# Kernel optimization log

Measured on AMD Instinct MI355X. Metric: run time of the kernel, lower is better.

Reference implementation:

```python
import jax, jax.numpy as jnp
import numpy as np

O, T, DIN, H, DOUT = 50000, 500000, 128, 256, 128


def setup_inputs() -> dict:
    key = jax.random.key(0)
    ks = jax.random.split(key, 12)
    s = 0.05
    return {
        "obj_vecs": jax.random.normal(ks[0], (O, DIN), jnp.float32),
        "pred_vecs": jax.random.normal(ks[1], (T, DIN), jnp.float32),
        "edges": jax.random.randint(ks[2], (T, 2), 0, O, jnp.int64),
        "w1a": jax.random.normal(ks[3], (3 * DIN, H), jnp.float32) * s,
        "b1a": jax.random.normal(ks[4], (H,), jnp.float32) * s,
        "w1b": jax.random.normal(ks[5], (H, 2 * H + DOUT), jnp.float32) * s,
        "b1b": jax.random.normal(ks[6], (2 * H + DOUT,), jnp.float32) * s,
        "w2a": jax.random.normal(ks[7], (H, H), jnp.float32) * s,
        "b2a": jax.random.normal(ks[8], (H,), jnp.float32) * s,
        "w2b": jax.random.normal(ks[9], (H, DOUT), jnp.float32) * s,
        "b2b": jax.random.normal(ks[10], (DOUT,), jnp.float32) * s,
    }


def reference(obj_vecs, pred_vecs, edges, w1a, b1a, w1b, b1b, w2a, b2a, w2b, b2b):
    n_obj = obj_vecs.shape[0]
    h_dim = w2a.shape[0]
    d_out = w2b.shape[1]
    s_idx = edges[:, 0]
    o_idx = edges[:, 1]
    # gather subject/object node features, concat with predicate: [T, 3*Din]
    cur_t = jnp.concatenate([obj_vecs[s_idx], pred_vecs, obj_vecs[o_idx]], axis=1)
    # edge MLP (net1): Linear-ReLU-Linear-ReLU -> [T, 2H + Dout]
    new_t = jax.nn.relu(jax.nn.relu(cur_t @ w1a + b1a) @ w1b + b1b)
    new_s = new_t[:, :h_dim]
    new_p = new_t[:, h_dim:h_dim + d_out]
    new_o = new_t[:, h_dim + d_out:]
    # scatter-add pooling back to nodes, both endpoints
    idx = jnp.concatenate([s_idx, o_idx])
    vals = jnp.concatenate([new_s, new_o], axis=0)
    pooled = jax.ops.segment_sum(vals, idx, num_segments=n_obj)
    # avg pooling: divide by per-node incidence count (clamped to >= 1)
    counts = jax.ops.segment_sum(jnp.ones(idx.shape[0], obj_vecs.dtype), idx,
                                 num_segments=n_obj)
    pooled = pooled / jnp.clip(counts, 1.0)[:, None]
    # node MLP (net2)
    new_obj = jax.nn.relu(jax.nn.relu(pooled @ w2a + b2a) @ w2b + b2b)
    return new_obj, new_p
```

## Files before the change

kernel.cpp:

```cpp
#include <hip/hip_runtime.h>


using f32x4 = __attribute__((ext_vector_type(4))) float;
using s16x8 = __attribute__((ext_vector_type(8))) short;
typedef unsigned short u16x8 __attribute__((ext_vector_type(8)));

#define VMCNT4  asm volatile("s_waitcnt vmcnt(4)" ::: "memory")
#define VMCNT8  asm volatile("s_waitcnt vmcnt(8)" ::: "memory")
#define VMCNT16 asm volatile("s_waitcnt vmcnt(16)" ::: "memory")
#define VMCNT20 asm volatile("s_waitcnt vmcnt(20)" ::: "memory")
#define VMCNT36 asm volatile("s_waitcnt vmcnt(36)" ::: "memory")
#define LGKM0   asm volatile("s_waitcnt lgkmcnt(0)" ::: "memory")
#define BAR     __builtin_amdgcn_s_barrier()
#define SCHEDB  __builtin_amdgcn_sched_barrier(0)

static __device__ __forceinline__ unsigned short f2b(float f) {
    unsigned int u = __float_as_uint(f);
    unsigned int r = (u + 0x7fffu + ((u >> 16) & 1u)) >> 16;
    return (unsigned short)r;
}

static __device__ __forceinline__ unsigned f2bpk(float lo, float hi) {
    unsigned r;
    asm("v_cvt_pk_bf16_f32 %0, %1, %2" : "=v"(r) : "v"(lo), "v"(hi));
    return r;
}

static __device__ __forceinline__ float b2f(unsigned short b) {
    return __uint_as_float(((unsigned)b) << 16);
}

static __device__ __forceinline__ unsigned swz(unsigned row, unsigned byteoff) {
    return byteoff ^ ((row & 7u) << 4);
}

static __device__ __forceinline__ void gload_lds16(const unsigned short* g, unsigned short* l) {
    __builtin_amdgcn_global_load_lds(
        (const __attribute__((address_space(1))) unsigned int*)g,
        (__attribute__((address_space(3))) unsigned int*)l,
        16, 0, 0);
}

#define PREP_ELEMS (98304 + 163840 + 65536 + 32768)

__global__ void prep_count_kernel(const float* __restrict__ w1a, const float* __restrict__ w1b,
                                  const float* __restrict__ w2a, const float* __restrict__ w2b,
                                  unsigned short* __restrict__ w1aT, unsigned short* __restrict__ w1bT,
                                  unsigned short* __restrict__ w2aT, unsigned short* __restrict__ w2bT,
                                  const int* __restrict__ edges, int* __restrict__ cnt,
                                  int* __restrict__ slotS, int* __restrict__ slotO, int T) {
    int t = blockIdx.x * blockDim.x + threadIdx.x;
    if (t >= PREP_ELEMS) {
        int e = t - PREP_ELEMS;
        if (e < T) {
            slotS[e] = atomicAdd(&cnt[edges[2 * (long long)e]], 1);
            slotO[e] = atomicAdd(&cnt[edges[2 * (long long)e + 1]], 1);
        }
        return;
    }
    if (t < 6 * 16384) {
        int kt = t >> 14;
        int rem = t & 16383; int c = rem >> 6, kk = rem & 63;
        unsigned byte = ((unsigned)(c * 128 + kk * 2)) ^ ((c & 7u) << 4);
        *(unsigned short*)((char*)w1aT + (size_t)kt * 32768 + byte) =
            f2b(w1a[(size_t)(kt * 64 + kk) * 256 + c]);
        return;
    }
    t -= 98304;
    if (t < 10 * 16384) {
        int tile = t >> 14; int nc = tile >> 1, kh = tile & 1;
        int rem = t & 16383; int c = rem >> 7, kk = rem & 127;
        unsigned byte = ((unsigned)(c * 256 + kk * 2)) ^ ((c & 7u) << 4);
        *(unsigned short*)((char*)w1bT + (size_t)tile * 32768 + byte) =
            f2b(w1b[(size_t)(kh * 128 + kk) * 640 + nc * 128 + c]);
        return;
    }
    t -= 163840;
    if (t < 65536) { int n = t >> 8, k = t & 255; w2aT[t] = f2b(w2a[k * 256 + n]); return; }
    t -= 65536;
    if (t < 32768) { int n = t >> 8, k = t & 255; w2bT[t] = f2b(w2b[k * 128 + n]); return; }
}

__global__ void scan_kernel(const int* __restrict__ cnt, int* __restrict__ rowptr, int O) {
    __shared__ int sc[1024];
    const int tid = threadIdx.x;
    const int per = (O + 1023) >> 10;
    const int base = tid * per;
    int s = 0;
    for (int i = 0; i < per; ++i) { int j = base + i; if (j < O) s += cnt[j]; }
    sc[tid] = s;
    __syncthreads();
    for (int d = 1; d < 1024; d <<= 1) {
        int v = (tid >= d) ? sc[tid - d] : 0;
        __syncthreads();
        sc[tid] += v;
        __syncthreads();
    }
    int off = sc[tid] - s;
    for (int i = 0; i < per; ++i) {
        int j = base + i;
        if (j < O) { rowptr[j] = off; off += cnt[j]; }
    }
    if (tid == 0) rowptr[O] = sc[1023];
}

__global__ __launch_bounds__(512, 2) void edge_mlp(
    const float* __restrict__ obj, const float* __restrict__ pred,
    const int* __restrict__ edges,
    const unsigned short* __restrict__ w1aT, const float* __restrict__ b1a,
    const unsigned short* __restrict__ w1bT, const float* __restrict__ b1b,
    const int* __restrict__ slotS, const int* __restrict__ slotO,
    const int* __restrict__ rowptr,
    unsigned short* __restrict__ edgeout, float* __restrict__ outP, int T) {
    const int m0 = blockIdx.x * 128;
    const int tid = threadIdx.x;
    const int lane = tid & 63, wid = tid >> 6;
    const int wm = wid >> 2, wn = wid & 3;
    const bool evenL = ((lane & 1) == 0);

    __shared__ unsigned short U[81920];
    char* const ldsb = (char*)U;
    char* const bbase = ldsb + 65536;

    bool okR[4][4];
    #pragma unroll
    for (int mi = 0; mi < 4; ++mi)
        #pragma unroll
        for (int rr = 0; rr < 4; ++rr)
            okR[mi][rr] = (m0 + wm * 64 + mi * 16 + ((lane >> 4) << 2) + rr) < T;

    int slotSr[4][2], slotOr[4][2];
    #pragma unroll
    for (int mi = 0; mi < 4; ++mi)
        #pragma unroll
        for (int k = 0; k < 2; ++k) {
            int rsel = evenL ? k : 2 + k;
            int e = m0 + wm * 64 + mi * 16 + ((lane >> 4) << 2) + rsel;
            if (e >= T) e = T - 1;
            int si = edges[2 * (long long)e];
            int oi = edges[2 * (long long)e + 1];
            slotSr[mi][k] = slotS[e] + rowptr[si];
            slotOr[mi][k] = slotO[e] + rowptr[oi];
        }

    const int r = tid >> 2;
    const int q = tid & 3;
    int e_r = m0 + r; if (e_r >= T) e_r = T - 1;
    const int sIdx_r = edges[2 * (long long)e_r];
    const int oIdx_r = edges[2 * (long long)e_r + 1];

    float bias1[4], bias2[5][2];
    #pragma unroll
    for (int nj = 0; nj < 4; ++nj) bias1[nj] = b1a[wn * 64 + nj * 16 + (lane & 15)];
    #pragma unroll
    for (int nc = 0; nc < 5; ++nc)
        #pragma unroll
        for (int nj = 0; nj < 2; ++nj)
            bias2[nc][nj] = b1b[nc * 128 + wn * 32 + nj * 16 + (lane & 15)];

    #pragma unroll
    for (int mi = 0; mi < 4; ++mi)
        #pragma unroll
        for (int k = 0; k < 2; ++k)
            asm volatile("" :: "v"(slotSr[mi][k]), "v"(slotOr[mi][k]));
    #pragma unroll
    for (int nj = 0; nj < 4; ++nj) asm volatile("" :: "v"(bias1[nj]));
    #pragma unroll
    for (int nc = 0; nc < 5; ++nc)
        #pragma unroll
        for (int nj = 0; nj < 2; ++nj) asm volatile("" :: "v"(bias2[nc][nj]));
    asm volatile("" :: "v"((float)sIdx_r), "v"((float)oIdx_r));
    SCHEDB;

    auto aSrc = [&](int kt) -> const float4* {
        const float* s;
        if (kt < 2)      s = obj  + (long long)sIdx_r * 128 + kt * 64;
        else if (kt < 4) s = pred + (long long)e_r   * 128 + (kt - 2) * 64;
        else             s = obj  + (long long)oIdx_r * 128 + (kt - 4) * 64;
        return (const float4*)s;
    };

    auto tp = [&](int i) -> const unsigned short* {
        return (i < 6) ? (w1aT + (size_t)i * 16384) : (w1bT + (size_t)(i - 6) * 16384);
    };

    auto stage32 = [&](const unsigned short* gt, char* bb) {
        #pragma unroll
        for (int rr4 = 0; rr4 < 4; ++rr4) {
            unsigned off = wid * 4096u + rr4 * 1024u;
            gload_lds16((const unsigned short*)((const char*)gt + off + lane * 16u),
                        (unsigned short*)(bb + off));
        }
    };

    auto writeA = [&](const float4* ap, char* ab) {
        #pragma unroll
        for (int i = 0; i < 4; ++i) {
            float4 v = ap[i];
            uint2 pk;
            pk.x = f2bpk(v.x, v.y);
            pk.y = f2bpk(v.z, v.w);
            unsigned byte = (r * 128u + q * 32u + i * 8u) ^ ((r & 7u) << 4);
            *(uint2*)(ab + byte) = pk;
        }
    };

    f32x4 acc1[4][4];
    #pragma unroll
    for (int a = 0; a < 4; ++a)
        #pragma unroll
        for (int b = 0; b < 4; ++b) acc1[a][b] = f32x4{0.f, 0.f, 0.f, 0.f};

    auto mfma1 = [&](const char* ab, const char* bb) {
        #pragma unroll
        for (int ks = 0; ks < 2; ++ks) {
            const unsigned kk = ks * 32u + ((lane >> 4) << 3);
            s16x8 af[4];
            #pragma unroll
            for (int mi = 0; mi < 4; ++mi) {
                unsigned row = wm * 64u + mi * 16u + (lane & 15);
                af[mi] = *(const s16x8*)(ab + ((row * 128u + kk * 2u) ^ ((row & 7u) << 4)));
            }
            #pragma unroll
            for (int nj = 0; nj < 4; ++nj) {
                unsigned c = wn * 64u + nj * 16u + (lane & 15);
                s16x8 bf = *(const s16x8*)(bb + ((c * 128u + kk * 2u) ^ ((c & 7u) << 4)));
                #pragma unroll
                for (int mi = 0; mi < 4; ++mi)
                    acc1[mi][nj] = __builtin_amdgcn_mfma_f32_16x16x32_bf16(af[mi], bf, acc1[mi][nj], 0, 0, 0);
            }
        }
    };

    float4 ap[4];
    {
        const float4* s4 = aSrc(0);
        #pragma unroll
        for (int i = 0; i < 4; ++i) ap[i] = s4[q * 4 + i];
    }
    writeA(ap, ldsb);
    stage32(tp(0), bbase);
    stage32(tp(1), bbase + 32768);
    {
        const float4* s4 = aSrc(1);
        #pragma unroll
        for (int i = 0; i < 4; ++i) ap[i] = s4[q * 4 + i];
    }
    VMCNT8;
    LGKM0; BAR; SCHEDB;

    #pragma unroll
    for (int s = 0; s < 6; ++s) {
        stage32(tp(s + 2), bbase + ((s + 2) % 3) * 32768);
        __builtin_amdgcn_s_setprio(1);
        mfma1(ldsb + (s & 1) * 16384, bbase + (s % 3) * 32768);
        __builtin_amdgcn_s_setprio(0);
        VMCNT4;
        if (s < 5) {
            writeA(ap, ldsb + ((s + 1) & 1) * 16384);
            if (s < 4) {
                const float4* s4 = aSrc(s + 2);
                #pragma unroll
                for (int i = 0; i < 4; ++i) ap[i] = s4[q * 4 + i];
            }
        }
        LGKM0; BAR; SCHEDB;
    }

    #pragma unroll
    for (int nj = 0; nj < 4; ++nj) {
        unsigned col = wn * 64u + nj * 16u + (lane & 15);
        #pragma unroll
        for (int mi = 0; mi < 4; ++mi) {
            float r0 = fmaxf(acc1[mi][nj][0] + bias1[nj], 0.f);
            float r1 = fmaxf(acc1[mi][nj][1] + bias1[nj], 0.f);
            float r2 = fmaxf(acc1[mi][nj][2] + bias1[nj], 0.f);
            float r3 = fmaxf(acc1[mi][nj][3] + bias1[nj], 0.f);
            unsigned p01 = f2bpk(r0, r1);
            unsigned p23 = f2bpk(r2, r3);
            unsigned rowb = wm * 64u + mi * 16u + ((lane >> 4) << 2);
            *(unsigned short*)(ldsb + ((rowb * 512u + col * 2u) ^ ((rowb & 7u) << 4))) = (unsigned short)p01;
            *(unsigned short*)(ldsb + (((rowb + 1) * 512u + col * 2u) ^ (((rowb + 1) & 7u) << 4))) = (unsigned short)(p01 >> 16);
            *(unsigned short*)(ldsb + (((rowb + 2) * 512u + col * 2u) ^ (((rowb + 2) & 7u) << 4))) = (unsigned short)p23;
            *(unsigned short*)(ldsb + (((rowb + 3) * 512u + col * 2u) ^ (((rowb + 3) & 7u) << 4))) = (unsigned short)(p23 >> 16);
        }
    }
    LGKM0; BAR; SCHEDB;

    #pragma unroll
    for (int nc = 0; nc < 5; ++nc) {
        f32x4 acc2[4][2];
        #pragma unroll
        for (int a = 0; a < 4; ++a)
            #pragma unroll
            for (int b = 0; b < 2; ++b) acc2[a][b] = f32x4{0.f, 0.f, 0.f, 0.f};

        #pragma unroll
        for (int kh = 0; kh < 2; ++kh) {
            const int s = 6 + nc * 2 + kh;
            if (s + 2 <= 15) stage32(tp(s + 2), bbase + ((s + 2) % 3) * 32768);
            const char* bb = bbase + (s % 3) * 32768;
            __builtin_amdgcn_s_setprio(1);
            #pragma unroll
            for (int ks = 0; ks < 4; ++ks) {
                const unsigned kkB = ks * 32u + ((lane >> 4) << 3);
                const unsigned kkH = (kh * 128u) + kkB;
                s16x8 af[4];
                #pragma unroll
                for (int mi = 0; mi < 4; ++mi) {
                    unsigned row = wm * 64u + mi * 16u + (lane & 15);
                    af[mi] = *(const s16x8*)(ldsb + ((row * 512u + kkH * 2u) ^ ((row & 7u) << 4)));
                }
                #pragma unroll
                for (int nj = 0; nj < 2; ++nj) {
                    unsigned c = wn * 32u + nj * 16u + (lane & 15);
                    s16x8 bf = *(const s16x8*)(bb + ((c * 256u + kkB * 2u) ^ ((c & 7u) << 4)));
                    #pragma unroll
                    for (int mi = 0; mi < 4; ++mi)
                        acc2[mi][nj] = __builtin_amdgcn_mfma_f32_16x16x32_bf16(af[mi], bf, acc2[mi][nj], 0, 0, 0);
                }
            }
            __builtin_amdgcn_s_setprio(0);

            if (kh == 0) {
                if (s == 6)       { VMCNT4; }
                else if (s == 12) { VMCNT36; }
                else if (s == 14) { VMCNT16; }
                else              { VMCNT20; }
                LGKM0; BAR; SCHEDB;
            }
        }

        if (nc == 2) {
            #pragma unroll
            for (int nj = 0; nj < 2; ++nj) {
                int col = 2 * 128 + wn * 32 + nj * 16 + (lane & 15);
                #pragma unroll
                for (int mi = 0; mi < 4; ++mi)
                    #pragma unroll
                    for (int rr = 0; rr < 4; ++rr) {
                        int row = wm * 64 + mi * 16 + ((lane >> 4) << 2) + rr;
                        if (okR[mi][rr]) {
                            float v = acc2[mi][nj][rr] + bias2[2][nj];
                            v = v > 0.f ? v : 0.f;
                            outP[(long long)(m0 + row) * 128 + (col - 256)] = v;
                        }
                    }
            }
            VMCNT36;
            LGKM0; BAR; SCHEDB;
        } else {
            #pragma unroll
            for (int nj = 0; nj < 2; ++nj) {
                int col = nc * 128 + wn * 32 + nj * 16 + (lane & 15);
                int pc = (nc < 2) ? col : (col - 384);
                int pcb = (lane & 1) ? (pc - 1) : pc;
                #pragma unroll
                for (int mi = 0; mi < 4; ++mi) {
                    float vv[4];
                    #pragma unroll
                    for (int rr = 0; rr < 4; ++rr) {
                        float v = acc2[mi][nj][rr] + bias2[nc][nj];
                        vv[rr] = v > 0.f ? v : 0.f;
                    }
                    float nb0 = __shfl_xor(vv[0], 1);
                    float nb1 = __shfl_xor(vv[1], 1);
                    float nb2 = __shfl_xor(vv[2], 1);
                    float nb3 = __shfl_xor(vv[3], 1);
                    #pragma unroll
                    for (int k = 0; k < 2; ++k) {
                        float lo = evenL ? (k ? vv[1] : vv[0]) : (k ? nb3 : nb2);
                        float hi = evenL ? (k ? nb1 : nb0) : (k ? vv[3] : vv[2]);
                        int rsel = evenL ? k : 2 + k;
                        if (okR[mi][rsel]) {
                            int slot = (nc < 2) ? slotSr[mi][k] : slotOr[mi][k];
                            unsigned pk = f2bpk(lo, hi);
                            *(unsigned*)(edgeout + (size_t)slot * 256 + pcb) = pk;
                        }
                    }
                }
            }
            if (nc < 4) {
                VMCNT20;
                LGKM0; BAR; SCHEDB;
            }
        }
    }
}

__global__ __launch_bounds__(256, 3) void obj_mlp(
    const unsigned short* __restrict__ edgeout, const int* __restrict__ rowptr,
    const unsigned short* __restrict__ w2aT, const float* __restrict__ b2a,
    const unsigned short* __restrict__ w2bT, const float* __restrict__ b2b,
    float* __restrict__ outObj, int O) {
    const int m0 = blockIdx.x * 64;
    const int tid = threadIdx.x;
    const int lane = tid & 63, wid = tid >> 6;
    const int wm = wid >> 1, wn = wid & 1;

    __shared__ unsigned short Abuf[64 * 256];

    for (int it = 0; it < 16; ++it) {
        const int row = it * 4 + wid;
        const int oI = m0 + row;
        float ax = 0.f, ay = 0.f, az = 0.f, aw = 0.f;
        float bx = 0.f, by = 0.f, bz = 0.f, bw = 0.f;
        int n = 0;
        if (oI < O) {
            const int beg = rowptr[oI];
            n = rowptr[oI + 1] - beg;
            const unsigned short* base = edgeout + (size_t)beg * 256 + lane * 4;
            int i = 0;
            for (; i + 7 < n; i += 8) {
                ushort4 v0 = *(const ushort4*)(base + (size_t)(i    ) * 256);
                ushort4 v1 = *(const ushort4*)(base + (size_t)(i + 1) * 256);
                ushort4 v2 = *(const ushort4*)(base + (size_t)(i + 2) * 256);
                ushort4 v3 = *(const ushort4*)(base + (size_t)(i + 3) * 256);
                ushort4 v4 = *(const ushort4*)(base + (size_t)(i + 4) * 256);
                ushort4 v5 = *(const ushort4*)(base + (size_t)(i + 5) * 256);
                ushort4 v6 = *(const ushort4*)(base + (size_t)(i + 6) * 256);
                ushort4 v7 = *(const ushort4*)(base + (size_t)(i + 7) * 256);
                ax += b2f(v0.x); ay += b2f(v0.y); az += b2f(v0.z); aw += b2f(v0.w);
                bx += b2f(v1.x); by += b2f(v1.y); bz += b2f(v1.z); bw += b2f(v1.w);
                ax += b2f(v2.x); ay += b2f(v2.y); az += b2f(v2.z); aw += b2f(v2.w);
                bx += b2f(v3.x); by += b2f(v3.y); bz += b2f(v3.z); bw += b2f(v3.w);
                ax += b2f(v4.x); ay += b2f(v4.y); az += b2f(v4.z); aw += b2f(v4.w);
                bx += b2f(v5.x); by += b2f(v5.y); bz += b2f(v5.z); bw += b2f(v5.w);
                ax += b2f(v6.x); ay += b2f(v6.y); az += b2f(v6.z); aw += b2f(v6.w);
                bx += b2f(v7.x); by += b2f(v7.y); bz += b2f(v7.z); bw += b2f(v7.w);
            }
            for (; i < n; ++i) {
                ushort4 v0 = *(const ushort4*)(base + (size_t)i * 256);
                ax += b2f(v0.x); ay += b2f(v0.y); az += b2f(v0.z); aw += b2f(v0.w);
            }
        }
        float inv = 1.f / fmaxf((float)n, 1.f);
        uint2 pk;
        pk.x = f2bpk((ax + bx) * inv, (ay + by) * inv);
        pk.y = f2bpk((az + bz) * inv, (aw + bw) * inv);
        unsigned byte = ((unsigned)row * 512u + (unsigned)lane * 8u) ^ (((unsigned)row & 7u) << 4);
        *(uint2*)((char*)Abuf + byte) = pk;
    }
    __syncthreads();

    f32x4 acc1[2][2][4];
    #pragma unroll
    for (int a = 0; a < 2; ++a)
        #pragma unroll
        for (int b = 0; b < 2; ++b)
            #pragma unroll
            for (int c = 0; c < 4; ++c) acc1[a][b][c] = f32x4{0.f, 0.f, 0.f, 0.f};
    #pragma unroll
    for (int ks = 0; ks < 8; ++ks) {
        const int klane = ks * 32 + ((lane >> 4) << 3);
        s16x8 af[2];
        #pragma unroll
        for (int mi = 0; mi < 2; ++mi) {
            int row = wm * 32 + mi * 16 + (lane & 15);
            af[mi] = *(const s16x8*)((const char*)Abuf + swz(row, row * 512u + klane * 2u));
        }
        #pragma unroll
        for (int nb = 0; nb < 2; ++nb)
            #pragma unroll
            for (int nj = 0; nj < 4; ++nj) {
                int col = nb * 128 + wn * 64 + nj * 16 + (lane & 15);
                s16x8 bf = *(const s16x8*)(w2aT + (long long)col * 256 + klane);
                #pragma unroll
                for (int mi = 0; mi < 2; ++mi)
                    acc1[nb][mi][nj] = __builtin_amdgcn_mfma_f32_16x16x32_bf16(af[mi], bf, acc1[nb][mi][nj], 0, 0, 0);
            }
    }
    __syncthreads();

    #pragma unroll
    for (int nb = 0; nb < 2; ++nb)
        #pragma unroll
        for (int nj = 0; nj < 4; ++nj) {
            int col = nb * 128 + wn * 64 + nj * 16 + (lane & 15);
            float bias = b2a[col];
            #pragma unroll
            for (int mi = 0; mi < 2; ++mi) {
                float r0 = fmaxf(acc1[nb][mi][nj][0] + bias, 0.f);
                float r1 = fmaxf(acc1[nb][mi][nj][1] + bias, 0.f);
                float r2 = fmaxf(acc1[nb][mi][nj][2] + bias, 0.f);
                float r3 = fmaxf(acc1[nb][mi][nj][3] + bias, 0.f);
                unsigned p01 = f2bpk(r0, r1);
                unsigned p23 = f2bpk(r2, r3);
                int rowb = wm * 32 + mi * 16 + ((lane >> 4) << 2);
                *(unsigned short*)((char*)Abuf + swz(rowb, rowb * 512u + col * 2u)) = (unsigned short)p01;
                *(unsigned short*)((char*)Abuf + swz(rowb + 1, (rowb + 1) * 512u + col * 2u)) = (unsigned short)(p01 >> 16);
                *(unsigned short*)((char*)Abuf + swz(rowb + 2, (rowb + 2) * 512u + col * 2u)) = (unsigned short)p23;
                *(unsigned short*)((char*)Abuf + swz(rowb + 3, (rowb + 3) * 512u + col * 2u)) = (unsigned short)(p23 >> 16);
            }
        }
    __syncthreads();

    f32x4 acc2[2][4];
    #pragma unroll
    for (int b = 0; b < 2; ++b)
        #pragma unroll
        for (int c = 0; c < 4; ++c) acc2[b][c] = f32x4{0.f, 0.f, 0.f, 0.f};
    #pragma unroll
    for (int ks = 0; ks < 8; ++ks) {
        const int klane = ks * 32 + ((lane >> 4) << 3);
        s16x8 af[2];
        #pragma unroll
        for (int mi = 0; mi < 2; ++mi) {
            int row = wm * 32 + mi * 16 + (lane & 15);
            af[mi] = *(const s16x8*)((const char*)Abuf + swz(row, row * 512u + klane * 2u));
        }
        #pragma unroll
        for (int nj = 0; nj < 4; ++nj) {
            int col = wn * 64 + nj * 16 + (lane & 15);
            s16x8 bf = *(const s16x8*)(w2bT + (long long)col * 256 + klane);
            #pragma unroll
            for (int mi = 0; mi < 2; ++mi)
                acc2[mi][nj] = __builtin_amdgcn_mfma_f32_16x16x32_bf16(af[mi], bf, acc2[mi][nj], 0, 0, 0);
        }
    }

    #pragma unroll
    for (int nj = 0; nj < 4; ++nj) {
        int col = wn * 64 + nj * 16 + (lane & 15);
        float bias = b2b[col];
        #pragma unroll
        for (int mi = 0; mi < 2; ++mi)
            #pragma unroll
            for (int rr = 0; rr < 4; ++rr) {
                int row = wm * 32 + mi * 16 + ((lane >> 4) << 2) + rr;
                int o = m0 + row;
                if (o < O) {
                    float v = acc2[mi][nj][rr] + bias;
                    v = v > 0.f ? v : 0.f;
                    outObj[(long long)o * 128 + col] = v;
                }
            }
    }
}

extern "C" void kernel_launch(void* const* d_in, const int* in_sizes, int n_in,
                              void* d_out, int out_size, void* d_ws, size_t ws_size,
                              hipStream_t stream) {
    const float* obj  = (const float*)d_in[0];
    const float* pred = (const float*)d_in[1];
    const int*   edges = (const int*)d_in[2];
    const float* w1a = (const float*)d_in[3];
    const float* b1a = (const float*)d_in[4];
    const float* w1b = (const float*)d_in[5];
    const float* b1b = (const float*)d_in[6];
    const float* w2a = (const float*)d_in[7];
    const float* b2a = (const float*)d_in[8];
    const float* w2b = (const float*)d_in[9];
    const float* b2b = (const float*)d_in[10];

    const int O = in_sizes[0] / 128;
    const int T = in_sizes[1] / 128;

    auto al = [](size_t x) { return (x + 255) & ~(size_t)255; };
    const size_t szEdgeout = (size_t)2 * T * 256 * 2;
    const size_t szCnt     = (size_t)O * 4;
    const size_t szRow     = (size_t)(O + 1) * 4;
    const size_t szSlot    = (size_t)T * 4;

    size_t off = 0;
    char* ws = (char*)d_ws;
    unsigned short* edgeout = (unsigned short*)(ws + off); off += al(szEdgeout);
    int* cnt    = (int*)(ws + off); off += al(szCnt);
    int* rowptr = (int*)(ws + off); off += al(szRow);
    int* slotS  = (int*)(ws + off); off += al(szSlot);
    int* slotO  = (int*)(ws + off); off += al(szSlot);
    unsigned short* w1aT = (unsigned short*)(ws + off); off += (size_t)6 * 16384 * 2;
    unsigned short* w1bT = (unsigned short*)(ws + off); off += (size_t)10 * 16384 * 2;
    unsigned short* w2aT = (unsigned short*)(ws + off); off += (size_t)256 * 256 * 2;
    unsigned short* w2bT = (unsigned short*)(ws + off);

    float* outObj = (float*)d_out;
    float* outP   = (float*)d_out + (size_t)O * 128;

    hipMemsetAsync(cnt, 0, szCnt, stream);
    const int totalT = PREP_ELEMS + T;
    prep_count_kernel<<<(totalT + 255) / 256, 256, 0, stream>>>(
        w1a, w1b, w2a, w2b, w1aT, w1bT, w2aT, w2bT, edges, cnt, slotS, slotO, T);
    scan_kernel<<<1, 1024, 0, stream>>>(cnt, rowptr, O);
    edge_mlp<<<(T + 127) / 128, 512, 0, stream>>>(obj, pred, edges, w1aT, b1a, w1bT, b1b,
                                                  slotS, slotO, rowptr, edgeout, outP, T);
    obj_mlp<<<(O + 63) / 64, 256, 0, stream>>>(edgeout, rowptr, w2aT, b2a, w2bT, b2b, outObj, O);
}
```

Baseline: 880.5 us.

## Halve edge MLP tile to 64 rows with 4 waves and finer K staging

The edge MLP block shrinks from 128 rows and 8 waves to 64 rows and 4 waves. Weight tiles are re-laid out as 16KB chunks with half the K depth, so the pipeline runs 32 stages instead of 16, with new wait counts at each step. Shared memory use drops from about 160KB to 80KB, which is meant to let more blocks stay resident and overlap gathers. In exchange, each weight tile is reused across half as many rows, so weight traffic and barrier overhead per edge go up.

```diff
diff --git a/kernel.cpp b/kernel.cpp
--- a/kernel.cpp
+++ b/kernel.cpp
@@ -5,9 +5,9 @@
 using s16x8 = __attribute__((ext_vector_type(8))) short;
 typedef unsigned short u16x8 __attribute__((ext_vector_type(8)));
 
+#define VMCNT0  asm volatile("s_waitcnt vmcnt(0)" ::: "memory")
 #define VMCNT4  asm volatile("s_waitcnt vmcnt(4)" ::: "memory")
 #define VMCNT8  asm volatile("s_waitcnt vmcnt(8)" ::: "memory")
-#define VMCNT16 asm volatile("s_waitcnt vmcnt(16)" ::: "memory")
 #define VMCNT20 asm volatile("s_waitcnt vmcnt(20)" ::: "memory")
 #define VMCNT36 asm volatile("s_waitcnt vmcnt(36)" ::: "memory")
 #define LGKM0   asm volatile("s_waitcnt lgkmcnt(0)" ::: "memory")
@@ -58,21 +58,21 @@
         }
         return;
     }
-    if (t < 6 * 16384) {
-        int kt = t >> 14;
-        int rem = t & 16383; int c = rem >> 6, kk = rem & 63;
+    if (t < 12 * 8192) {
+        int kt = t >> 13;
+        int rem = t & 8191; int c = rem >> 5, kk = rem & 31;
+        unsigned byte = ((unsigned)(c * 64 + kk * 2)) ^ ((c & 7u) << 4);
+        *(unsigned short*)((char*)w1aT + (size_t)kt * 16384 + byte) =
+            f2b(w1a[(size_t)(kt * 32 + kk) * 256 + c]);
+        return;
+    }
+    t -= 98304;
+    if (t < 20 * 8192) {
+        int tile = t >> 13; int nc = tile >> 2, kh = tile & 3;
+        int rem = t & 8191; int c = rem >> 6, kk = rem & 63;
         unsigned byte = ((unsigned)(c * 128 + kk * 2)) ^ ((c & 7u) << 4);
-        *(unsigned short*)((char*)w1aT + (size_t)kt * 32768 + byte) =
-            f2b(w1a[(size_t)(kt * 64 + kk) * 256 + c]);
-        return;
-    }
-    t -= 98304;
-    if (t < 10 * 16384) {
-        int tile = t >> 14; int nc = tile >> 1, kh = tile & 1;
-        int rem = t & 16383; int c = rem >> 7, kk = rem & 127;
-        unsigned byte = ((unsigned)(c * 256 + kk * 2)) ^ ((c & 7u) << 4);
-        *(unsigned short*)((char*)w1bT + (size_t)tile * 32768 + byte) =
-            f2b(w1b[(size_t)(kh * 128 + kk) * 640 + nc * 128 + c]);
+        *(unsigned short*)((char*)w1bT + (size_t)tile * 16384 + byte) =
+            f2b(w1b[(size_t)(kh * 64 + kk) * 640 + nc * 128 + c]);
         return;
     }
     t -= 163840;
@@ -104,7 +104,7 @@
     if (tid == 0) rowptr[O] = sc[1023];
 }
 
-__global__ __launch_bounds__(512, 2) void edge_mlp(
+__global__ __launch_bounds__(256, 2) void edge_mlp(
     const float* __restrict__ obj, const float* __restrict__ pred,
     const int* __restrict__ edges,
     const unsigned short* __restrict__ w1aT, const float* __restrict__ b1a,
@@ -112,22 +112,22 @@
     const int* __restrict__ slotS, const int* __restrict__ slotO,
     const int* __restrict__ rowptr,
     unsigned short* __restrict__ edgeout, float* __restrict__ outP, int T) {
-    const int m0 = blockIdx.x * 128;
+    const int m0 = blockIdx.x * 64;
     const int tid = threadIdx.x;
     const int lane = tid & 63, wid = tid >> 6;
-    const int wm = wid >> 2, wn = wid & 3;
+    const int wn = wid;
     const bool evenL = ((lane & 1) == 0);
 
-    __shared__ unsigned short U[81920];
+    __shared__ unsigned short U[40960];
     char* const ldsb = (char*)U;
-    char* const bbase = ldsb + 65536;
+    char* const bbase = ldsb + 32768;
 
     bool okR[4][4];
     #pragma unroll
     for (int mi = 0; mi < 4; ++mi)
         #pragma unroll
         for (int rr = 0; rr < 4; ++rr)
-            okR[mi][rr] = (m0 + wm * 64 + mi * 16 + ((lane >> 4) << 2) + rr) < T;
+            okR[mi][rr] = (m0 + mi * 16 + ((lane >> 4) << 2) + rr) < T;
 
     int slotSr[4][2], slotOr[4][2];
     #pragma unroll
@@ -135,7 +135,7 @@
         #pragma unroll
         for (int k = 0; k < 2; ++k) {
             int rsel = evenL ? k : 2 + k;
-            int e = m0 + wm * 64 + mi * 16 + ((lane >> 4) << 2) + rsel;
+            int e = m0 + mi * 16 + ((lane >> 4) << 2) + rsel;
             if (e >= T) e = T - 1;
             int si = edges[2 * (long long)e];
             int oi = edges[2 * (long long)e + 1];
@@ -172,19 +172,19 @@
     asm volatile("" :: "v"((float)sIdx_r), "v"((float)oIdx_r));
     SCHEDB;
 
-    auto aSrc = [&](int kt) -> const float4* {
+    auto aSrc = [&](int j) -> const float4* {
         const float* s;
-        if (kt < 2)      s = obj  + (long long)sIdx_r * 128 + kt * 64;
-        else if (kt < 4) s = pred + (long long)e_r   * 128 + (kt - 2) * 64;
-        else             s = obj  + (long long)oIdx_r * 128 + (kt - 4) * 64;
+        if (j < 2)      s = obj  + (long long)sIdx_r * 128 + j * 64;
+        else if (j < 4) s = pred + (long long)e_r   * 128 + (j - 2) * 64;
+        else            s = obj  + (long long)oIdx_r * 128 + (j - 4) * 64;
         return (const float4*)s;
     };
 
     auto tp = [&](int i) -> const unsigned short* {
-        return (i < 6) ? (w1aT + (size_t)i * 16384) : (w1bT + (size_t)(i - 6) * 16384);
+        return (i < 12) ? (w1aT + (size_t)i * 8192) : (w1bT + (size_t)(i - 12) * 8192);
     };
 
-    auto stage32 = [&](const unsigned short* gt, char* bb) {
+    auto stage16 = [&](const unsigned short* gt, char* bb) {
         #pragma unroll
         for (int rr4 = 0; rr4 < 4; ++rr4) {
             unsigned off = wid * 4096u + rr4 * 1024u;
@@ -211,24 +211,22 @@
         #pragma unroll
         for (int b = 0; b < 4; ++b) acc1[a][b] = f32x4{0.f, 0.f, 0.f, 0.f};
 
-    auto mfma1 = [&](const char* ab, const char* bb) {
-        #pragma unroll
-        for (int ks = 0; ks < 2; ++ks) {
-            const unsigned kk = ks * 32u + ((lane >> 4) << 3);
-            s16x8 af[4];
-            #pragma unroll
-            for (int mi = 0; mi < 4; ++mi) {
-                unsigned row = wm * 64u + mi * 16u + (lane & 15);
-                af[mi] = *(const s16x8*)(ab + ((row * 128u + kk * 2u) ^ ((row & 7u) << 4)));
-            }
-            #pragma unroll
-            for (int nj = 0; nj < 4; ++nj) {
-                unsigned c = wn * 64u + nj * 16u + (lane & 15);
-                s16x8 bf = *(const s16x8*)(bb + ((c * 128u + kk * 2u) ^ ((c & 7u) << 4)));
-                #pragma unroll
-                for (int mi = 0; mi < 4; ++mi)
-                    acc1[mi][nj] = __builtin_amdgcn_mfma_f32_16x16x32_bf16(af[mi], bf, acc1[mi][nj], 0, 0, 0);
-            }
+    auto mfma1 = [&](const char* ab, const char* bb, unsigned koff) {
+        const unsigned kkA = koff + ((lane >> 4) << 3);
+        const unsigned kkB = ((lane >> 4) << 3);
+        s16x8 af[4];
+        #pragma unroll
+        for (int mi = 0; mi < 4; ++mi) {
+            unsigned row = mi * 16u + (lane & 15);
+            af[mi] = *(const s16x8*)(ab + ((row * 128u + kkA * 2u) ^ ((row & 7u) << 4)));
+        }
+        #pragma unroll
+        for (int nj = 0; nj < 4; ++nj) {
+            unsigned c = wn * 64u + nj * 16u + (lane & 15);
+            s16x8 bf = *(const s16x8*)(bb + ((c * 64u + kkB * 2u) ^ ((c & 7u) << 4)));
+            #pragma unroll
+            for (int mi = 0; mi < 4; ++mi)
+                acc1[mi][nj] = __builtin_amdgcn_mfma_f32_16x16x32_bf16(af[mi], bf, acc1[mi][nj], 0, 0, 0);
         }
     };
 
@@ -239,8 +237,8 @@
         for (int i = 0; i < 4; ++i) ap[i] = s4[q * 4 + i];
     }
     writeA(ap, ldsb);
-    stage32(tp(0), bbase);
-    stage32(tp(1), bbase + 32768);
+    stage16(tp(0), bbase);
+    stage16(tp(1), bbase + 16384);
     {
         const float4* s4 = aSrc(1);
         #pragma unroll
@@ -250,19 +248,25 @@
     LGKM0; BAR; SCHEDB;
 
     #pragma unroll
-    for (int s = 0; s < 6; ++s) {
-        stage32(tp(s + 2), bbase + ((s + 2) % 3) * 32768);
+    for (int s = 0; s < 12; ++s) {
+        stage16(tp(s + 2), bbase + ((s + 2) % 3) * 16384);
         __builtin_amdgcn_s_setprio(1);
-        mfma1(ldsb + (s & 1) * 16384, bbase + (s % 3) * 32768);
+        mfma1(ldsb + ((s >> 1) & 1) * 8192, bbase + (s % 3) * 16384, (s & 1) * 32u);
         __builtin_amdgcn_s_setprio(0);
-        VMCNT4;
-        if (s < 5) {
-            writeA(ap, ldsb + ((s + 1) & 1) * 16384);
-            if (s < 4) {
-                const float4* s4 = aSrc(s + 2);
+        if ((s & 1) == 1 && s <= 9) {
+            VMCNT8;
+            writeA(ap, ldsb + (((s >> 1) + 1) & 1) * 8192);
+            if (s <= 7) {
+                const float4* s4 = aSrc((s >> 1) + 2);
                 #pragma unroll
                 for (int i = 0; i < 4; ++i) ap[i] = s4[q * 4 + i];
-            }
+                VMCNT8;
+            } else {
+                VMCNT4;
+            }
+        } else {
+            if (s <= 8) { VMCNT8; }
+            else        { VMCNT4; }
         }
         LGKM0; BAR; SCHEDB;
     }
@@ -278,7 +282,7 @@
             float r3 = fmaxf(acc1[mi][nj][3] + bias1[nj], 0.f);
             unsigned p01 = f2bpk(r0, r1);
             unsigned p23 = f2bpk(r2, r3);
-            unsigned rowb = wm * 64u + mi * 16u + ((lane >> 4) << 2);
+            unsigned rowb = mi * 16u + ((lane >> 4) << 2);
             *(unsigned short*)(ldsb + ((rowb * 512u + col * 2u) ^ ((rowb & 7u) << 4))) = (unsigned short)p01;
             *(unsigned short*)(ldsb + (((rowb + 1) * 512u + col * 2u) ^ (((rowb + 1) & 7u) << 4))) = (unsigned short)(p01 >> 16);
             *(unsigned short*)(ldsb + (((rowb + 2) * 512u + col * 2u) ^ (((rowb + 2) & 7u) << 4))) = (unsigned short)p23;
@@ -287,103 +291,99 @@
     }
     LGKM0; BAR; SCHEDB;
 
-    #pragma unroll
-    for (int nc = 0; nc < 5; ++nc) {
-        f32x4 acc2[4][2];
-        #pragma unroll
-        for (int a = 0; a < 4; ++a)
-            #pragma unroll
-            for (int b = 0; b < 2; ++b) acc2[a][b] = f32x4{0.f, 0.f, 0.f, 0.f};
-
-        #pragma unroll
-        for (int kh = 0; kh < 2; ++kh) {
-            const int s = 6 + nc * 2 + kh;
-            if (s + 2 <= 15) stage32(tp(s + 2), bbase + ((s + 2) % 3) * 32768);
-            const char* bb = bbase + (s % 3) * 32768;
-            __builtin_amdgcn_s_setprio(1);
-            #pragma unroll
-            for (int ks = 0; ks < 4; ++ks) {
-                const unsigned kkB = ks * 32u + ((lane >> 4) << 3);
-                const unsigned kkH = (kh * 128u) + kkB;
-                s16x8 af[4];
+    f32x4 acc2[4][2];
+    #pragma unroll
+    for (int s = 12; s < 32; ++s) {
+        const int nc = (s - 12) >> 2;
+        const int kh = (s - 12) & 3;
+        if (kh == 0) {
+            #pragma unroll
+            for (int a = 0; a < 4; ++a)
                 #pragma unroll
-                for (int mi = 0; mi < 4; ++mi) {
-                    unsigned row = wm * 64u + mi * 16u + (lane & 15);
-                    af[mi] = *(const s16x8*)(ldsb + ((row * 512u + kkH * 2u) ^ ((row & 7u) << 4)));
-                }
+                for (int b = 0; b < 2; ++b) acc2[a][b] = f32x4{0.f, 0.f, 0.f, 0.f};
+        }
+        if (s + 2 <= 31) stage16(tp(s + 2), bbase + ((s + 2) % 3) * 16384);
+        const char* bb = bbase + (s % 3) * 16384;
+        __builtin_amdgcn_s_setprio(1);
+        #pragma unroll
+        for (int ks = 0; ks < 2; ++ks) {
+            const unsigned kkB = ks * 32u + ((lane >> 4) << 3);
+            const unsigned kkH = kh * 64u + kkB;
+            s16x8 af[4];
+            #pragma unroll
+            for (int mi = 0; mi < 4; ++mi) {
+                unsigned row = mi * 16u + (lane & 15);
+                af[mi] = *(const s16x8*)(ldsb + ((row * 512u + kkH * 2u) ^ ((row & 7u) << 4)));
+            }
+            #pragma unroll
+            for (int nj = 0; nj < 2; ++nj) {
+                unsigned c = wn * 32u + nj * 16u + (lane & 15);
+                s16x8 bf = *(const s16x8*)(bb + ((c * 128u + kkB * 2u) ^ ((c & 7u) << 4)));
+                #pragma unroll
+                for (int mi = 0; mi < 4; ++mi)
+                    acc2[mi][nj] = __builtin_amdgcn_mfma_f32_16x16x32_bf16(af[mi], bf, acc2[mi][nj], 0, 0, 0);
+            }
+        }
+        __builtin_amdgcn_s_setprio(0);
+
+        if (kh == 3) {
+            if (nc == 2) {
                 #pragma unroll
                 for (int nj = 0; nj < 2; ++nj) {
-                    unsigned c = wn * 32u + nj * 16u + (lane & 15);
-                    s16x8 bf = *(const s16x8*)(bb + ((c * 256u + kkB * 2u) ^ ((c & 7u) << 4)));
+                    int col = 2 * 128 + wn * 32 + nj * 16 + (lane & 15);
                     #pragma unroll
                     for (int mi = 0; mi < 4; ++mi)
-                        acc2[mi][nj] = __builtin_amdgcn_mfma_f32_16x16x32_bf16(af[mi], bf, acc2[mi][nj], 0, 0, 0);
+                        #pragma unroll
+                        for (int rr = 0; rr < 4; ++rr) {
+                            int row = mi * 16 + ((lane >> 4) << 2) + rr;
+                            if (okR[mi][rr]) {
+                                float v = acc2[mi][nj][rr] + bias2[2][nj];
+                                v = v > 0.f ? v : 0.f;
+                                outP[(long long)(m0 + row) * 128 + (col - 256)] = v;
+                            }
+                        }
                 }
-            }
-            __builtin_amdgcn_s_setprio(0);
-
-            if (kh == 0) {
-                if (s == 6)       { VMCNT4; }
-                else if (s == 12) { VMCNT36; }
-                else if (s == 14) { VMCNT16; }
-                else              { VMCNT20; }
-                LGKM0; BAR; SCHEDB;
-            }
-        }
-
-        if (nc == 2) {
-            #pragma unroll
-            for (int nj = 0; nj < 2; ++nj) {
-                int col = 2 * 128 + wn * 32 + nj * 16 + (lane & 15);
+            } else {
                 #pragma unroll
-                for (int mi = 0; mi < 4; ++mi)
+                for (int nj = 0; nj < 2; ++nj) {
+                    int col = nc * 128 + wn * 32 + nj * 16 + (lane & 15);
+                    int pc = (nc < 2) ? col : (col - 384);
+                    int pcb = (lane & 1) ? (pc - 1) : pc;
                     #pragma unroll
-                    for (int rr = 0; rr < 4; ++rr) {
-                        int row = wm * 64 + mi * 16 + ((lane >> 4) << 2) + rr;
-                        if (okR[mi][rr]) {
-                            float v = acc2[mi][nj][rr] + bias2[2][nj];
-                            v = v > 0.f ? v : 0.f;
-                            outP[(long long)(m0 + row) * 128 + (col - 256)] = v;
+                    for (int mi = 0; mi < 4; ++mi) {
+                        float vv[4];
+                        #pragma unroll
+                        for (int rr = 0; rr < 4; ++rr) {
+                            float v = acc2[mi][nj][rr] + bias2[nc][nj];
+                            vv[rr] = v > 0.f ? v : 0.f;
                         }
-                    }
-            }
-            VMCNT36;
-            LGKM0; BAR; SCHEDB;
-        } else {
-            #pragma unroll
-            for (int nj = 0; nj < 2; ++nj) {
-                int col = nc * 128 + wn * 32 + nj * 16 + (lane & 15);
-                int pc = (nc < 2) ? col : (col - 384);
-                int pcb = (lane & 1) ? (pc - 1) : pc;
-                #pragma unroll
-                for (int mi = 0; mi < 4; ++mi) {
-                    float vv[4];
-                    #pragma unroll
-                    for (int rr = 0; rr < 4; ++rr) {
-                        float v = acc2[mi][nj][rr] + bias2[nc][nj];
-                        vv[rr] = v > 0.f ? v : 0.f;
-                    }
-                    float nb0 = __shfl_xor(vv[0], 1);
-                    float nb1 = __shfl_xor(vv[1], 1);
-                    float nb2 = __shfl_xor(vv[2], 1);
-                    float nb3 = __shfl_xor(vv[3], 1);
-                    #pragma unroll
-                    for (int k = 0; k < 2; ++k) {
-                        float lo = evenL ? (k ? vv[1] : vv[0]) : (k ? nb3 : nb2);
-                        float hi = evenL ? (k ? nb1 : nb0) : (k ? vv[3] : vv[2]);
-                        int rsel = evenL ? k : 2 + k;
-                        if (okR[mi][rsel]) {
-                            int slot = (nc < 2) ? slotSr[mi][k] : slotOr[mi][k];
-                            unsigned pk = f2bpk(lo, hi);
-                            *(unsigned*)(edgeout + (size_t)slot * 256 + pcb) = pk;
+                        float nb0 = __shfl_xor(vv[0], 1);
+                        float nb1 = __shfl_xor(vv[1], 1);
+                        float nb2 = __shfl_xor(vv[2], 1);
+                        float nb3 = __shfl_xor(vv[3], 1);
+                        #pragma unroll
+                        for (int k = 0; k < 2; ++k) {
+                            float lo = evenL ? (k ? vv[1] : vv[0]) : (k ? nb3 : nb2);
+                            float hi = evenL ? (k ? nb1 : nb0) : (k ? vv[3] : vv[2]);
+                            int rsel = evenL ? k : 2 + k;
+                            if (okR[mi][rsel]) {
+                                int slot = (nc < 2) ? slotSr[mi][k] : slotOr[mi][k];
+                                unsigned pk = f2bpk(lo, hi);
+                                *(unsigned*)(edgeout + (size_t)slot * 256 + pcb) = pk;
+                            }
                         }
                     }
                 }
             }
-            if (nc < 4) {
-                VMCNT20;
-                LGKM0; BAR; SCHEDB;
-            }
+        }
+
+        if (s < 31) {
+            if (s == 30)                                           { VMCNT0; }
+            else if (s == 15 || s == 16 || s == 19 || s == 20 ||
+                     s == 27 || s == 28)                           { VMCNT20; }
+            else if (s == 23 || s == 24)                           { VMCNT36; }
+            else                                                   { VMCNT4; }
+            LGKM0; BAR; SCHEDB;
         }
     }
 }
@@ -569,8 +569,8 @@
     int* rowptr = (int*)(ws + off); off += al(szRow);
     int* slotS  = (int*)(ws + off); off += al(szSlot);
     int* slotO  = (int*)(ws + off); off += al(szSlot);
-    unsigned short* w1aT = (unsigned short*)(ws + off); off += (size_t)6 * 16384 * 2;
-    unsigned short* w1bT = (unsigned short*)(ws + off); off += (size_t)10 * 16384 * 2;
+    unsigned short* w1aT = (unsigned short*)(ws + off); off += (size_t)12 * 8192 * 2;
+    unsigned short* w1bT = (unsigned short*)(ws + off); off += (size_t)20 * 8192 * 2;
     unsigned short* w2aT = (unsigned short*)(ws + off); off += (size_t)256 * 256 * 2;
     unsigned short* w2bT = (unsigned short*)(ws + off);
 
@@ -582,7 +582,7 @@
     prep_count_kernel<<<(totalT + 255) / 256, 256, 0, stream>>>(
         w1a, w1b, w2a, w2b, w1aT, w1bT, w2aT, w2bT, edges, cnt, slotS, slotO, T);
     scan_kernel<<<1, 1024, 0, stream>>>(cnt, rowptr, O);
-    edge_mlp<<<(T + 127) / 128, 512, 0, stream>>>(obj, pred, edges, w1aT, b1a, w1bT, b1b,
-                                                  slotS, slotO, rowptr, edgeout, outP, T);
+    edge_mlp<<<(T + 63) / 64, 256, 0, stream>>>(obj, pred, edges, w1aT, b1a, w1bT, b1b,
+                                                slotS, slotO, rowptr, edgeout, outP, T);
     obj_mlp<<<(O + 63) / 64, 256, 0, stream>>>(edgeout, rowptr, w2aT, b2a, w2bT, b2b, outObj, O);
 }
```

Result: no change. 890.9 us (+1.2%).
